# Performance work log

Hardware: AMD Instinct MI355X
Metric: run time of the kernel (lower is better)

Reference implementation:

```python
import jax, jax.numpy as jnp
import numpy as np

N, E, D, H = 50000, 500000, 128, 4
C = D // H
EPS = 1e-5


def _layer_norm(x, g, b):
    mu = jnp.mean(x, axis=-1, keepdims=True)
    var = jnp.mean((x - mu) ** 2, axis=-1, keepdims=True)
    return (x - mu) * jax.lax.rsqrt(var + EPS) * g + b


def setup_inputs() -> dict:
    key = jax.random.key(0)
    ks = jax.random.split(key, 20)
    f = lambda i, shape: jax.random.normal(ks[i], shape, dtype=jnp.float32) * 0.05
    return {
        "x": f(0, (N, D)),
        "edge_index": jax.random.randint(ks[1], (2, E), 0, N),
        "w_gcn": f(2, (D, D)), "b_gcn": f(3, (D,)),
        "wq": f(4, (D, D)), "bq": f(5, (D,)),
        "wk": f(6, (D, D)), "bk": f(7, (D,)),
        "wv": f(8, (D, D)), "bv": f(9, (D,)),
        "w_skip": f(10, (D, D)), "b_skip": f(11, (D,)),
        "w_beta": f(12, (3 * D, 1)),
        "g1": jnp.ones((D,), jnp.float32), "b1": jnp.zeros((D,), jnp.float32),
        "g2": jnp.ones((D,), jnp.float32), "b2": jnp.zeros((D,), jnp.float32),
        "w_rel": f(13, (D, 2 * D)), "w_root": f(14, (2 * D, D)),
        "local_w": jnp.ones((1,), jnp.float32), "global_w": jnp.ones((1,), jnp.float32),
    }


def reference(x, edge_index, w_gcn, b_gcn, wq, bq, wk, bk, wv, bv,
              w_skip, b_skip, w_beta, g1, b1, g2, b2, w_rel, w_root,
              local_w, global_w):
    src, dst = edge_index[0], edge_index[1]

    # ---- GCNConv (add_self_loops=False, symmetric norm) ----
    xw = x @ w_gcn                                   # [N, D]
    deg = jax.ops.segment_sum(jnp.ones((E,), x.dtype), dst, num_segments=N)
    dinv = jnp.where(deg > 0, jax.lax.rsqrt(jnp.maximum(deg, 1.0)), 0.0)
    coef = dinv[src] * dinv[dst]                     # [E]
    local_out = jax.ops.segment_sum(coef[:, None] * xw[src], dst, num_segments=N) + b_gcn

    # ---- TransformerConv (heads=4, concat=True, beta=True) ----
    q = (x @ wq + bq).reshape(N, H, C)
    k = (x @ wk + bk).reshape(N, H, C)
    v = (x @ wv + bv).reshape(N, H, C)
    alpha = jnp.sum(q[dst] * k[src], axis=-1) / jnp.sqrt(jnp.float32(C))  # [E, H]
    m = jax.ops.segment_max(alpha, dst, num_segments=N)
    m = jnp.where(jnp.isfinite(m), m, 0.0)
    a = jnp.exp(alpha - m[dst])
    s = jax.ops.segment_sum(a, dst, num_segments=N)
    attn = a / jnp.maximum(s[dst], 1e-16)            # [E, H] segment softmax over in-edges
    agg = jax.ops.segment_sum(attn[..., None] * v[src], dst, num_segments=N)
    out_g = agg.reshape(N, D)
    x_r = x @ w_skip + b_skip
    beta = jax.nn.sigmoid(jnp.concatenate([out_g, x_r, out_g - x_r], axis=-1) @ w_beta)
    global_out = beta * x_r + (1.0 - beta) * out_g

    # ---- combine + norm + FFN ----
    h = local_w * local_out + global_w * global_out
    h = _layer_norm(h + h, g1, b1)
    out = jax.nn.relu(h @ w_rel) @ w_root
    out = _layer_norm(out + h, g2, b2)
    return out
```

## Files before the change

### kernel.cpp

```cpp
#include <hip/hip_runtime.h>
#include <math.h>

#define D 128
#define EPSV 1e-5f

typedef unsigned short ushort_t;
typedef unsigned char uchar_t;
typedef __attribute__((ext_vector_type(8))) short short8v;
typedef __attribute__((ext_vector_type(4))) float f32x4;
typedef __attribute__((ext_vector_type(2))) float f32x2;

__device__ __forceinline__ float bf2f(unsigned u) {
    return __uint_as_float(u << 16);
}
__device__ __forceinline__ ushort_t f2bf(float f) {
    unsigned u = __float_as_uint(f);
    unsigned r = (u + 0x7fffu + ((u >> 16) & 1u)) >> 16;
    return (ushort_t)r;
}
__device__ __forceinline__ float bfp(uint4 v, int i) {
    unsigned w = (&v.x)[i >> 1];
    return bf2f((i & 1) ? (w >> 16) : (w & 0xffffu));
}

#define UNPACK8_FP8(u, o) { \
    f32x2 _a = __builtin_amdgcn_cvt_pk_f32_fp8((int)(u).x, false); \
    f32x2 _b = __builtin_amdgcn_cvt_pk_f32_fp8((int)(u).x, true);  \
    f32x2 _c = __builtin_amdgcn_cvt_pk_f32_fp8((int)(u).y, false); \
    f32x2 _d = __builtin_amdgcn_cvt_pk_f32_fp8((int)(u).y, true);  \
    o[0] = _a.x; o[1] = _a.y; o[2] = _b.x; o[3] = _b.y;            \
    o[4] = _c.x; o[5] = _c.y; o[6] = _d.x; o[7] = _d.y; }

__device__ __forceinline__ unsigned bf4_to_fp8x4(unsigned w0, unsigned w1) {
    int u = __builtin_amdgcn_cvt_pk_fp8_f32(bf2f(w0 & 0xffffu), bf2f(w0 >> 16), 0, false);
    u = __builtin_amdgcn_cvt_pk_fp8_f32(bf2f(w1 & 0xffffu), bf2f(w1 >> 16), u, true);
    return (unsigned)u;
}

__global__ __launch_bounds__(256)
void proj_gemm(const float* __restrict__ x,
               const ushort_t* __restrict__ Bt,
               const float* __restrict__ bias,
               uchar_t* __restrict__ pack, ushort_t* __restrict__ qb,
               ushort_t* __restrict__ xrb, int M)
{
    __shared__ ushort_t Cs[128 * 136];
    const int tid = threadIdx.x, lane = tid & 63, wid = tid >> 6;
    const int wr = wid >> 1, wc = wid & 1;
    const int R0 = blockIdx.x * 128;
    const int cbeg = blockIdx.y ? 3 : 0;
    const int cend = blockIdx.y ? 5 : 3;

    short8v av[4][4];
    #pragma unroll
    for (int r = 0; r < 4; ++r) {
        int gr = R0 + wr * 64 + r * 16 + (lane & 15);
        if (gr >= M) gr = M - 1;
        const float* xrow = x + (size_t)gr * 128 + (lane >> 4) * 8;
        #pragma unroll
        for (int ks = 0; ks < 4; ++ks) {
            float4 lo = *reinterpret_cast<const float4*>(xrow + ks * 32);
            float4 hi = *reinterpret_cast<const float4*>(xrow + ks * 32 + 4);
            short8v a;
            a[0] = (short)f2bf(lo.x); a[1] = (short)f2bf(lo.y);
            a[2] = (short)f2bf(lo.z); a[3] = (short)f2bf(lo.w);
            a[4] = (short)f2bf(hi.x); a[5] = (short)f2bf(hi.y);
            a[6] = (short)f2bf(hi.z); a[7] = (short)f2bf(hi.w);
            av[r][ks] = a;
        }
    }

    for (int ct = cbeg; ct < cend; ++ct) {
        f32x4 acc[4][4] = {};
        #pragma unroll
        for (int ks = 0; ks < 4; ++ks) {
            short8v bv[4];
            #pragma unroll
            for (int c = 0; c < 4; ++c) {
                int col = ct * 128 + wc * 64 + c * 16 + (lane & 15);
                bv[c] = *reinterpret_cast<const short8v*>(
                    &Bt[(size_t)col * 128 + ks * 32 + (lane >> 4) * 8]);
            }
            #pragma unroll
            for (int r = 0; r < 4; ++r)
                #pragma unroll
                for (int c = 0; c < 4; ++c)
                    acc[r][c] = __builtin_amdgcn_mfma_f32_16x16x32_bf16(av[r][ks], bv[c], acc[r][c], 0, 0, 0);
        }
        __syncthreads();
        #pragma unroll
        for (int r = 0; r < 4; ++r) {
            int rowb = wr * 64 + r * 16 + (lane >> 4) * 4;
            #pragma unroll
            for (int i = 0; i < 4; ++i)
                #pragma unroll
                for (int c = 0; c < 4; ++c) {
                    int col = wc * 64 + c * 16 + (lane & 15);
                    Cs[(rowb + i) * 136 + col] = f2bf(acc[r][c][i] + bias[ct * 128 + col]);
                }
        }
        __syncthreads();
        if (ct == 1 || ct == 4) {
            #pragma unroll
            for (int it = 0; it < 8; ++it) {
                int linear = tid + it * 256;
                int row = linear >> 4, ch = linear & 15;
                int gr = R0 + row;
                if (gr < M) {
                    uint4 v = *reinterpret_cast<const uint4*>(&Cs[row * 136 + ch * 8]);
                    ushort_t* dst = (ct == 1) ? (qb + (size_t)gr * 128)
                                              : (xrb + (size_t)gr * 128);
                    *reinterpret_cast<uint4*>(dst + ch * 8) = v;
                }
            }
        } else {
            const int byteoff = (ct == 0) ? 256 : (ct == 2) ? 0 : 128;
            #pragma unroll
            for (int it = 0; it < 4; ++it) {
                int linear = tid + it * 256;
                int row = linear >> 3, ch = linear & 7;
                int gr = R0 + row;
                if (gr < M) {
                    uint4 lo = *reinterpret_cast<const uint4*>(&Cs[row * 136 + ch * 16]);
                    uint4 hi = *reinterpret_cast<const uint4*>(&Cs[row * 136 + ch * 16 + 8]);
                    uint4 o;
                    o.x = bf4_to_fp8x4(lo.x, lo.y);
                    o.y = bf4_to_fp8x4(lo.z, lo.w);
                    o.z = bf4_to_fp8x4(hi.x, hi.y);
                    o.w = bf4_to_fp8x4(hi.z, hi.w);
                    *reinterpret_cast<uint4*>(pack + (size_t)gr * 384 + byteoff + ch * 16) = o;
                }
            }
        }
    }
}

__device__ __forceinline__ int swz(int ch, int row) {
    return (ch & 24) | ((ch ^ row) & 7);
}

__global__ __launch_bounds__(256)
void ffn_fused(const ushort_t* __restrict__ hlnb,
               const ushort_t* __restrict__ wt_rel,
               const ushort_t* __restrict__ wt_root,
               const float* __restrict__ g2, const float* __restrict__ b2,
               float* __restrict__ outf, int M)
{
    __shared__ float smem[128 * 130];
    ushort_t* Hs = (ushort_t*)smem;
    const int tid = threadIdx.x, lane = tid & 63, wid = tid >> 6;
    const int wr = wid >> 1, wc = wid & 1;
    const int R0 = blockIdx.x * 128;

    short8v av[4][4];
    #pragma unroll
    for (int r = 0; r < 4; ++r) {
        int gr = R0 + wr * 64 + r * 16 + (lane & 15);
        if (gr >= M) gr = M - 1;
        #pragma unroll
        for (int ks = 0; ks < 4; ++ks)
            av[r][ks] = *reinterpret_cast<const short8v*>(
                &hlnb[(size_t)gr * 128 + ks * 32 + (lane >> 4) * 8]);
    }
    for (int ct = 0; ct < 2; ++ct) {
        f32x4 acc[4][4] = {};
        #pragma unroll
        for (int ks = 0; ks < 4; ++ks) {
            short8v bv[4];
            #pragma unroll
            for (int c = 0; c < 4; ++c) {
                int col = ct * 128 + wc * 64 + c * 16 + (lane & 15);
                bv[c] = *reinterpret_cast<const short8v*>(
                    &wt_rel[(size_t)col * 128 + ks * 32 + (lane >> 4) * 8]);
            }
            #pragma unroll
            for (int r = 0; r < 4; ++r)
                #pragma unroll
                for (int c = 0; c < 4; ++c)
                    acc[r][c] = __builtin_amdgcn_mfma_f32_16x16x32_bf16(av[r][ks], bv[c], acc[r][c], 0, 0, 0);
        }
        #pragma unroll
        for (int r = 0; r < 4; ++r) {
            int rowb = wr * 64 + r * 16 + (lane >> 4) * 4;
            #pragma unroll
            for (int i = 0; i < 4; ++i)
                #pragma unroll
                for (int c = 0; c < 4; ++c) {
                    int row = rowb + i;
                    int col = ct * 128 + wc * 64 + c * 16 + (lane & 15);
                    int ch = col >> 3, el = col & 7;
                    Hs[row * 256 + swz(ch, row) * 8 + el] = f2bf(fmaxf(acc[r][c][i], 0.f));
                }
        }
    }
    __syncthreads();

    f32x4 acc2[4][4] = {};
    #pragma unroll
    for (int ks = 0; ks < 8; ++ks) {
        short8v a2[4], bv[4];
        #pragma unroll
        for (int r = 0; r < 4; ++r) {
            int row = wr * 64 + r * 16 + (lane & 15);
            int ch = ks * 4 + (lane >> 4);
            a2[r] = *reinterpret_cast<const short8v*>(&Hs[row * 256 + swz(ch, row) * 8]);
        }
        #pragma unroll
        for (int c = 0; c < 4; ++c) {
            int col = wc * 64 + c * 16 + (lane & 15);
            bv[c] = *reinterpret_cast<const short8v*>(
                &wt_root[(size_t)col * 256 + ks * 32 + (lane >> 4) * 8]);
        }
        #pragma unroll
        for (int r = 0; r < 4; ++r)
            #pragma unroll
            for (int c = 0; c < 4; ++c)
                acc2[r][c] = __builtin_amdgcn_mfma_f32_16x16x32_bf16(a2[r], bv[c], acc2[r][c], 0, 0, 0);
    }
    __syncthreads();

    float* Cs = smem;
    #pragma unroll
    for (int r = 0; r < 4; ++r) {
        int rowb = wr * 64 + r * 16 + (lane >> 4) * 4;
        #pragma unroll
        for (int i = 0; i < 4; ++i)
            #pragma unroll
            for (int c = 0; c < 4; ++c)
                Cs[(rowb + i) * 130 + wc * 64 + c * 16 + (lane & 15)] = acc2[r][c][i];
    }
    __syncthreads();

    const float ga = g2[lane * 2], gb = g2[lane * 2 + 1];
    const float ba = b2[lane * 2], bb2 = b2[lane * 2 + 1];
    for (int rr = 0; rr < 32; ++rr) {
        int row = wid * 32 + rr;
        int gr = R0 + row;
        if (gr >= M) break;
        unsigned hu = *reinterpret_cast<const unsigned*>(&hlnb[(size_t)gr * 128 + lane * 2]);
        float t0 = Cs[row * 130 + lane * 2]     + bf2f(hu & 0xffffu);
        float t1 = Cs[row * 130 + lane * 2 + 1] + bf2f(hu >> 16);
        float ssum = t0 + t1;
        #pragma unroll
        for (int off = 1; off <= 32; off <<= 1) ssum += __shfl_xor(ssum, off);
        float mu = ssum * (1.f / 128.f);
        float dv0 = t0 - mu, dv1 = t1 - mu;
        float vsum = dv0 * dv0 + dv1 * dv1;
        #pragma unroll
        for (int off = 1; off <= 32; off <<= 1) vsum += __shfl_xor(vsum, off);
        float rs = rsqrtf(vsum * (1.f / 128.f) + EPSV);
        float2 o = make_float2(dv0 * rs * ga + ba, dv1 * rs * gb + bb2);
        *reinterpret_cast<float2*>(&outf[(size_t)gr * 128 + lane * 2]) = o;
    }
}

__global__ void pack_weights_kernel(const float* __restrict__ wg, const float* __restrict__ wq,
                                    const float* __restrict__ wk, const float* __restrict__ wv,
                                    const float* __restrict__ wsk,
                                    const float* __restrict__ bq, const float* __restrict__ bk,
                                    const float* __restrict__ bv, const float* __restrict__ bsk,
                                    const float* __restrict__ wrel, const float* __restrict__ wroot,
                                    ushort_t* __restrict__ wt_all, ushort_t* __restrict__ wt_rel,
                                    ushort_t* __restrict__ wt_root, float* __restrict__ bias_all)
{
    int i = blockIdx.x * 256 + threadIdx.x;
    if (i < 640 * 128) {
        int n = i >> 7, k = i & 127;
        const float* srcs[5] = {wg, wq, wk, wv, wsk};
        wt_all[i] = f2bf(srcs[n >> 7][k * 128 + (n & 127)]);
    } else if (i < 640 * 128 + 256 * 128) {
        int j = i - 640 * 128;
        int n = j >> 7, k = j & 127;
        wt_rel[j] = f2bf(wrel[k * 256 + n]);
    } else if (i < 640 * 128 + 256 * 128 + 128 * 256) {
        int j = i - (640 * 128 + 256 * 128);
        int n = j >> 8, k = j & 255;
        wt_root[j] = f2bf(wroot[k * 128 + n]);
    } else if (i < 640 * 128 + 256 * 128 + 128 * 256 + 640) {
        int n = i - (640 * 128 + 256 * 128 + 128 * 256);
        float b = 0.f;
        if (n >= 128) {
            const float* bs[4] = {bq, bk, bv, bsk};
            b = bs[(n - 128) >> 7][n & 127];
        }
        bias_all[n] = b;
    }
}

__global__ void deg_count_kernel(const int* __restrict__ dst, int* __restrict__ deg, int E)
{
    int e = blockIdx.x * blockDim.x + threadIdx.x;
    if (e < E) atomicAdd(&deg[dst[e]], 1);
}

__global__ __launch_bounds__(256)
void scan1_kernel(const int* __restrict__ deg, int* __restrict__ row_start,
                  int* __restrict__ bsum, int n)
{
    __shared__ int ws[4];
    const int t = threadIdx.x, lane = t & 63, wid = t >> 6;
    const int base = blockIdx.x * 1024 + t * 4;
    int v0 = 0, v1 = 0, v2 = 0, v3 = 0;
    if (base + 3 < n) {
        int4 q = *reinterpret_cast<const int4*>(&deg[base]);
        v0 = q.x; v1 = q.y; v2 = q.z; v3 = q.w;
    } else {
        if (base < n)     v0 = deg[base];
        if (base + 1 < n) v1 = deg[base + 1];
        if (base + 2 < n) v2 = deg[base + 2];
        if (base + 3 < n) v3 = deg[base + 3];
    }
    int tot = v0 + v1 + v2 + v3;
    int inc = tot;
    #pragma unroll
    for (int off = 1; off < 64; off <<= 1) {
        int y = __shfl_up(inc, off);
        if (lane >= off) inc += y;
    }
    if (lane == 63) ws[wid] = inc;
    __syncthreads();
    int woff = 0;
    for (int w = 0; w < wid; ++w) woff += ws[w];
    int excl = woff + inc - tot;
    if (base < n)     row_start[base]     = excl;
    if (base + 1 < n) row_start[base + 1] = excl + v0;
    if (base + 2 < n) row_start[base + 2] = excl + v0 + v1;
    if (base + 3 < n) row_start[base + 3] = excl + v0 + v1 + v2;
    if (t == 0) bsum[blockIdx.x] = ws[0] + ws[1] + ws[2] + ws[3];
}

__global__ __launch_bounds__(256)
void scan3_kernel(const int* __restrict__ deg, const int* __restrict__ bsum,
                  int* __restrict__ row_start, int* __restrict__ cursor,
                  float* __restrict__ dinv, int n, int E)
{
    __shared__ int boff_s;
    const int K = blockIdx.x >> 2;
    if (threadIdx.x == 0) {
        int s = 0;
        for (int j = 0; j < K; ++j) s += bsum[j];
        boff_s = s;
    }
    __syncthreads();
    int i = blockIdx.x * 256 + threadIdx.x;
    if (i < n) {
        int rs = row_start[i] + boff_s;
        row_start[i] = rs;
        cursor[i] = rs;
        int d = deg[i];
        dinv[i] = (d > 0) ? rsqrtf((float)d) : 0.f;
    }
    if (i == 0) row_start[n] = E;
}

__global__ void fill_kernel(const int* __restrict__ src, const int* __restrict__ dst,
                            int* __restrict__ cursor, int* __restrict__ csr_src, int E)
{
    int e = blockIdx.x * blockDim.x + threadIdx.x;
    if (e < E) {
        int d = dst[e];
        int pos = atomicAdd(&cursor[d], 1);
        csr_src[pos] = src[e];
    }
}

__global__ __launch_bounds__(256)
void edge_fused_kernel(const uchar_t* __restrict__ pack,
                       const ushort_t* __restrict__ qbf,
                       const ushort_t* __restrict__ xrbf,
                       const int* __restrict__ row_start,
                       const int* __restrict__ csr_src,
                       const float* __restrict__ dinv,
                       const float* __restrict__ b_gcn,
                       const float* __restrict__ w_beta,
                       const float* __restrict__ g1, const float* __restrict__ b1,
                       const float* __restrict__ local_w, const float* __restrict__ global_w,
                       ushort_t* __restrict__ hln_bf, int n)
{
    const int wid = threadIdx.x >> 6, lane = threadIdx.x & 63;
    const int node = blockIdx.x * 4 + wid;
    if (node >= n) return;
    const int slot = lane >> 4, li = lane & 15;
    const int d8 = li * 8;

    uint4 qu = *reinterpret_cast<const uint4*>(&qbf[(size_t)node * 128 + d8]);
    float q[8];
    #pragma unroll
    for (int i = 0; i < 8; ++i) q[i] = bfp(qu, i);

    const int e0 = row_start[node], e1 = row_start[node + 1];
    const float dn = dinv[node];
    const float scale = 0.17677669529663687f;

    float s = 0.f, va[8] = {}, ga[8] = {};

    for (int j = e0; j < e1; j += 4) {
        const int je = j + slot;
        const bool act = je < e1;
        const int sidx = act ? csr_src[je] : 0;
        const uchar_t* prow = pack + (size_t)sidx * 384;
        uint2 ku = *reinterpret_cast<const uint2*>(prow + d8);
        uint2 vu = *reinterpret_cast<const uint2*>(prow + 128 + d8);
        uint2 xu = *reinterpret_cast<const uint2*>(prow + 256 + d8);
        float kf[8], vf[8], xf[8];
        UNPACK8_FP8(ku, kf);
        UNPACK8_FP8(vu, vf);
        UNPACK8_FP8(xu, xf);
        float p = 0.f;
        #pragma unroll
        for (int i = 0; i < 8; ++i) p = fmaf(q[i], kf[i], p);
        p += __shfl_xor(p, 1);
        p += __shfl_xor(p, 2);
        float wgt = act ? __expf(p * scale) : 0.f;
        float c   = act ? dn * dinv[sidx] : 0.f;
        s += wgt;
        #pragma unroll
        for (int i = 0; i < 8; ++i) {
            va[i] = fmaf(wgt, vf[i], va[i]);
            ga[i] = fmaf(c,   xf[i], ga[i]);
        }
    }
    #pragma unroll
    for (int off = 16; off <= 32; off <<= 1) {
        s += __shfl_xor(s, off);
        #pragma unroll
        for (int i = 0; i < 8; ++i) {
            va[i] += __shfl_xor(va[i], off);
            ga[i] += __shfl_xor(ga[i], off);
        }
    }
    const float denom = fmaxf(s, 1e-16f);

    uint4 xru = *reinterpret_cast<const uint4*>(&xrbf[(size_t)node * 128 + d8]);
    float t[8];
    float part = 0.f;
    #pragma unroll
    for (int i = 0; i < 8; ++i) {
        float og = va[i] / denom;
        float xr = bfp(xru, i);
        float lo = ga[i] + b_gcn[d8 + i];
        part += og * w_beta[d8 + i] + xr * w_beta[128 + d8 + i]
              + (og - xr) * w_beta[256 + d8 + i];
        t[i] = lo;
        va[i] = og; ga[i] = xr;
    }
    #pragma unroll
    for (int off = 1; off <= 32; off <<= 1) part += __shfl_xor(part, off);
    const float beta = 1.f / (1.f + __expf(-part * 0.25f));

    const float lw = local_w[0], gw = global_w[0];
    float ssum = 0.f;
    #pragma unroll
    for (int i = 0; i < 8; ++i) {
        float go = beta * ga[i] + (1.f - beta) * va[i];
        t[i] = 2.f * (lw * t[i] + gw * go);
        ssum += t[i];
    }
    #pragma unroll
    for (int off = 1; off <= 32; off <<= 1) ssum += __shfl_xor(ssum, off);
    const float mu = ssum * (1.f / 512.f);
    float vsum = 0.f;
    #pragma unroll
    for (int i = 0; i < 8; ++i) { float d = t[i] - mu; vsum += d * d; }
    #pragma unroll
    for (int off = 1; off <= 32; off <<= 1) vsum += __shfl_xor(vsum, off);
    const float rs = rsqrtf(vsum * (1.f / 512.f) + EPSV);

    if (slot == 0) {
        uint4 o;
        #pragma unroll
        for (int i = 0; i < 4; ++i) {
            float o0 = (t[2*i]   - mu) * rs * g1[d8 + 2*i]   + b1[d8 + 2*i];
            float o1 = (t[2*i+1] - mu) * rs * g1[d8 + 2*i+1] + b1[d8 + 2*i+1];
            (&o.x)[i] = (unsigned)f2bf(o0) | ((unsigned)f2bf(o1) << 16);
        }
        *reinterpret_cast<uint4*>(&hln_bf[(size_t)node * 128 + d8]) = o;
    }
}

extern "C" void kernel_launch(void* const* d_in, const int* in_sizes, int n_in,
                              void* d_out, int out_size, void* d_ws, size_t ws_size,
                              hipStream_t stream)
{
    const float* x      = (const float*)d_in[0];
    const int*   ei     = (const int*)d_in[1];
    const float* w_gcn  = (const float*)d_in[2];
    const float* b_gcn  = (const float*)d_in[3];
    const float* wq     = (const float*)d_in[4];
    const float* bq     = (const float*)d_in[5];
    const float* wk     = (const float*)d_in[6];
    const float* bk     = (const float*)d_in[7];
    const float* wv     = (const float*)d_in[8];
    const float* bv     = (const float*)d_in[9];
    const float* w_skip = (const float*)d_in[10];
    const float* b_skip = (const float*)d_in[11];
    const float* w_beta = (const float*)d_in[12];
    const float* g1     = (const float*)d_in[13];
    const float* b1     = (const float*)d_in[14];
    const float* g2     = (const float*)d_in[15];
    const float* b2     = (const float*)d_in[16];
    const float* w_rel  = (const float*)d_in[17];
    const float* w_root = (const float*)d_in[18];
    const float* lw     = (const float*)d_in[19];
    const float* gw     = (const float*)d_in[20];

    const int N = in_sizes[0] / D;
    const int E = in_sizes[1] / 2;
    const int* src = ei;
    const int* dst = ei + E;

    char* wsb = (char*)d_ws;
    size_t off = 0;
    auto alloc = [&](size_t bytes) -> void* {
        void* p = wsb + off;
        off += (bytes + 255) & ~(size_t)255;
        return p;
    };
    uchar_t*  pack_kvx = (uchar_t*)alloc((size_t)N * 384);
    ushort_t* qb_bf    = (ushort_t*)alloc((size_t)N * 128 * 2);
    ushort_t* xr_bf    = (ushort_t*)alloc((size_t)N * 128 * 2);
    ushort_t* hln_bf   = (ushort_t*)alloc((size_t)N * 128 * 2);
    ushort_t* wt_all   = (ushort_t*)alloc(640 * 128 * 2);
    ushort_t* wt_rel   = (ushort_t*)alloc(256 * 128 * 2);
    ushort_t* wt_root  = (ushort_t*)alloc(128 * 256 * 2);
    float*    bias_all = (float*)alloc(640 * 4);
    int*      deg      = (int*)alloc((size_t)N * 4);
    int*      row_start= (int*)alloc((size_t)(N + 1) * 4);
    int*      cursor   = (int*)alloc((size_t)N * 4);
    int*      csr_src  = (int*)alloc((size_t)E * 4);
    float*    dinv     = (float*)alloc((size_t)N * 4);
    int*      bsum     = (int*)alloc(((size_t)(N + 1023) / 1024) * 4);

    float* out = (float*)d_out;
    const int SB = (N + 1023) / 1024;

    hipMemsetAsync(deg, 0, (size_t)N * sizeof(int), stream);
    deg_count_kernel<<<dim3((E + 255) / 256), dim3(256), 0, stream>>>(dst, deg, E);
    scan1_kernel<<<dim3(SB), dim3(256), 0, stream>>>(deg, row_start, bsum, N);
    scan3_kernel<<<dim3((N + 255) / 256), dim3(256), 0, stream>>>(
        deg, bsum, row_start, cursor, dinv, N, E);
    fill_kernel<<<dim3((E + 255) / 256), dim3(256), 0, stream>>>(src, dst, cursor, csr_src, E);

    pack_weights_kernel<<<dim3(579), dim3(256), 0, stream>>>(
        w_gcn, wq, wk, wv, w_skip, bq, bk, bv, b_skip, w_rel, w_root,
        wt_all, wt_rel, wt_root, bias_all);

    const int MB = (N + 127) / 128;
    proj_gemm<<<dim3(MB, 2), dim3(256), 0, stream>>>(
        x, wt_all, bias_all, pack_kvx, qb_bf, xr_bf, N);

    edge_fused_kernel<<<dim3((N + 3) / 4), dim3(256), 0, stream>>>(
        pack_kvx, qb_bf, xr_bf, row_start, csr_src, dinv, b_gcn, w_beta,
        g1, b1, lw, gw, hln_bf, N);

    ffn_fused<<<dim3(MB), dim3(256), 0, stream>>>(
        hln_bf, wt_rel, wt_root, g2, b2, out, N);
}
```

Measured before the change: 215.1 us.

## Prescale GCN features by source dinv and accumulate edges in packed fp16

Folds the source-side GCN normalisation dinv[src] into the projection epilogue, so the edge loop no longer gathers dinv per edge and applies dn once after aggregation. Stores q as fp16 and, when the builtin exists, converts fp8 to packed half2 and does the dot products and accumulation in fp16 packed math. Inactive lanes now point at a zeroed dummy row instead of row 0. The pack_weights launch is merged into the scan1 kernel to remove one launch. This trades accumulation precision (fp16 sums over many edges) for fewer instructions and fewer irregular loads.

```diff
diff --git a/kernel.cpp b/kernel.cpp
--- a/kernel.cpp
+++ b/kernel.cpp
@@ -9,6 +9,14 @@
 typedef __attribute__((ext_vector_type(8))) short short8v;
 typedef __attribute__((ext_vector_type(4))) float f32x4;
 typedef __attribute__((ext_vector_type(2))) float f32x2;
+typedef _Float16 half_t;
+typedef __attribute__((ext_vector_type(2))) _Float16 h2;
+
+#if __has_builtin(__builtin_amdgcn_cvt_pk_f16_fp8)
+#define HAVE_F16P 1
+#else
+#define HAVE_F16P 0
+#endif
 
 __device__ __forceinline__ float bf2f(unsigned u) {
     return __uint_as_float(u << 16);
@@ -21,6 +29,15 @@
 __device__ __forceinline__ float bfp(uint4 v, int i) {
     unsigned w = (&v.x)[i >> 1];
     return bf2f((i & 1) ? (w >> 16) : (w & 0xffffu));
+}
+
+__device__ __forceinline__ ushort_t qconv(float f) {
+#if HAVE_F16P
+    half_t h = (half_t)f;
+    return __builtin_bit_cast(ushort_t, h);
+#else
+    return f2bf(f);
+#endif
 }
 
 #define UNPACK8_FP8(u, o) { \
@@ -41,6 +58,7 @@
 void proj_gemm(const float* __restrict__ x,
                const ushort_t* __restrict__ Bt,
                const float* __restrict__ bias,
+               const float* __restrict__ dinv,
                uchar_t* __restrict__ pack, ushort_t* __restrict__ qb,
                ushort_t* __restrict__ xrb, int M)
 {
@@ -92,12 +110,21 @@
         for (int r = 0; r < 4; ++r) {
             int rowb = wr * 64 + r * 16 + (lane >> 4) * 4;
             #pragma unroll
-            for (int i = 0; i < 4; ++i)
+            for (int i = 0; i < 4; ++i) {
+                float sc = 1.f;
+                if (ct == 0) {
+                    int grow = R0 + rowb + i;
+                    if (grow >= M) grow = M - 1;
+                    sc = dinv[grow];
+                }
                 #pragma unroll
                 for (int c = 0; c < 4; ++c) {
                     int col = wc * 64 + c * 16 + (lane & 15);
-                    Cs[(rowb + i) * 136 + col] = f2bf(acc[r][c][i] + bias[ct * 128 + col]);
+                    float val = acc[r][c][i] + bias[ct * 128 + col];
+                    if (ct == 0) val *= sc;
+                    Cs[(rowb + i) * 136 + col] = (ct == 1) ? qconv(val) : f2bf(val);
                 }
+            }
         }
         __syncthreads();
         if (ct == 1 || ct == 4) {
@@ -254,36 +281,72 @@
     }
 }
 
-__global__ void pack_weights_kernel(const float* __restrict__ wg, const float* __restrict__ wq,
-                                    const float* __restrict__ wk, const float* __restrict__ wv,
-                                    const float* __restrict__ wsk,
-                                    const float* __restrict__ bq, const float* __restrict__ bk,
-                                    const float* __restrict__ bv, const float* __restrict__ bsk,
-                                    const float* __restrict__ wrel, const float* __restrict__ wroot,
-                                    ushort_t* __restrict__ wt_all, ushort_t* __restrict__ wt_rel,
-                                    ushort_t* __restrict__ wt_root, float* __restrict__ bias_all)
-{
-    int i = blockIdx.x * 256 + threadIdx.x;
-    if (i < 640 * 128) {
-        int n = i >> 7, k = i & 127;
-        const float* srcs[5] = {wg, wq, wk, wv, wsk};
-        wt_all[i] = f2bf(srcs[n >> 7][k * 128 + (n & 127)]);
-    } else if (i < 640 * 128 + 256 * 128) {
-        int j = i - 640 * 128;
-        int n = j >> 7, k = j & 127;
-        wt_rel[j] = f2bf(wrel[k * 256 + n]);
-    } else if (i < 640 * 128 + 256 * 128 + 128 * 256) {
-        int j = i - (640 * 128 + 256 * 128);
-        int n = j >> 8, k = j & 255;
-        wt_root[j] = f2bf(wroot[k * 128 + n]);
-    } else if (i < 640 * 128 + 256 * 128 + 128 * 256 + 640) {
-        int n = i - (640 * 128 + 256 * 128 + 128 * 256);
-        float b = 0.f;
-        if (n >= 128) {
-            const float* bs[4] = {bq, bk, bv, bsk};
-            b = bs[(n - 128) >> 7][n & 127];
-        }
-        bias_all[n] = b;
+__global__ __launch_bounds__(256)
+void scan1_packw_kernel(const int* __restrict__ deg, int* __restrict__ row_start,
+                        int* __restrict__ bsum, int n, int SB,
+                        const float* __restrict__ wg, const float* __restrict__ wq,
+                        const float* __restrict__ wk, const float* __restrict__ wv,
+                        const float* __restrict__ wsk,
+                        const float* __restrict__ bq, const float* __restrict__ bk,
+                        const float* __restrict__ bv, const float* __restrict__ bsk,
+                        const float* __restrict__ wrel, const float* __restrict__ wroot,
+                        ushort_t* __restrict__ wt_all, ushort_t* __restrict__ wt_rel,
+                        ushort_t* __restrict__ wt_root, float* __restrict__ bias_all)
+{
+    __shared__ int ws[4];
+    if ((int)blockIdx.x < SB) {
+        const int t = threadIdx.x, lane = t & 63, wid = t >> 6;
+        const int base = blockIdx.x * 1024 + t * 4;
+        int v0 = 0, v1 = 0, v2 = 0, v3 = 0;
+        if (base + 3 < n) {
+            int4 q = *reinterpret_cast<const int4*>(&deg[base]);
+            v0 = q.x; v1 = q.y; v2 = q.z; v3 = q.w;
+        } else {
+            if (base < n)     v0 = deg[base];
+            if (base + 1 < n) v1 = deg[base + 1];
+            if (base + 2 < n) v2 = deg[base + 2];
+            if (base + 3 < n) v3 = deg[base + 3];
+        }
+        int tot = v0 + v1 + v2 + v3;
+        int inc = tot;
+        #pragma unroll
+        for (int off = 1; off < 64; off <<= 1) {
+            int y = __shfl_up(inc, off);
+            if (lane >= off) inc += y;
+        }
+        if (lane == 63) ws[wid] = inc;
+        __syncthreads();
+        int woff = 0;
+        for (int w = 0; w < wid; ++w) woff += ws[w];
+        int excl = woff + inc - tot;
+        if (base < n)     row_start[base]     = excl;
+        if (base + 1 < n) row_start[base + 1] = excl + v0;
+        if (base + 2 < n) row_start[base + 2] = excl + v0 + v1;
+        if (base + 3 < n) row_start[base + 3] = excl + v0 + v1 + v2;
+        if (t == 0) bsum[blockIdx.x] = ws[0] + ws[1] + ws[2] + ws[3];
+    } else {
+        int i = (blockIdx.x - SB) * 256 + threadIdx.x;
+        if (i < 640 * 128) {
+            int c = i >> 7, k = i & 127;
+            const float* srcs[5] = {wg, wq, wk, wv, wsk};
+            wt_all[i] = f2bf(srcs[c >> 7][k * 128 + (c & 127)]);
+        } else if (i < 640 * 128 + 256 * 128) {
+            int j = i - 640 * 128;
+            int c = j >> 7, k = j & 127;
+            wt_rel[j] = f2bf(wrel[k * 256 + c]);
+        } else if (i < 640 * 128 + 256 * 128 + 128 * 256) {
+            int j = i - (640 * 128 + 256 * 128);
+            int c = j >> 8, k = j & 255;
+            wt_root[j] = f2bf(wroot[k * 128 + c]);
+        } else if (i < 640 * 128 + 256 * 128 + 128 * 256 + 640) {
+            int c = i - (640 * 128 + 256 * 128 + 128 * 256);
+            float b = 0.f;
+            if (c >= 128) {
+                const float* bs[4] = {bq, bk, bv, bsk};
+                b = bs[(c - 128) >> 7][c & 127];
+            }
+            bias_all[c] = b;
+        }
     }
 }
 
@@ -291,42 +354,6 @@
 {
     int e = blockIdx.x * blockDim.x + threadIdx.x;
     if (e < E) atomicAdd(&deg[dst[e]], 1);
-}
-
-__global__ __launch_bounds__(256)
-void scan1_kernel(const int* __restrict__ deg, int* __restrict__ row_start,
-                  int* __restrict__ bsum, int n)
-{
-    __shared__ int ws[4];
-    const int t = threadIdx.x, lane = t & 63, wid = t >> 6;
-    const int base = blockIdx.x * 1024 + t * 4;
-    int v0 = 0, v1 = 0, v2 = 0, v3 = 0;
-    if (base + 3 < n) {
-        int4 q = *reinterpret_cast<const int4*>(&deg[base]);
-        v0 = q.x; v1 = q.y; v2 = q.z; v3 = q.w;
-    } else {
-        if (base < n)     v0 = deg[base];
-        if (base + 1 < n) v1 = deg[base + 1];
-        if (base + 2 < n) v2 = deg[base + 2];
-        if (base + 3 < n) v3 = deg[base + 3];
-    }
-    int tot = v0 + v1 + v2 + v3;
-    int inc = tot;
-    #pragma unroll
-    for (int off = 1; off < 64; off <<= 1) {
-        int y = __shfl_up(inc, off);
-        if (lane >= off) inc += y;
-    }
-    if (lane == 63) ws[wid] = inc;
-    __syncthreads();
-    int woff = 0;
-    for (int w = 0; w < wid; ++w) woff += ws[w];
-    int excl = woff + inc - tot;
-    if (base < n)     row_start[base]     = excl;
-    if (base + 1 < n) row_start[base + 1] = excl + v0;
-    if (base + 2 < n) row_start[base + 2] = excl + v0 + v1;
-    if (base + 3 < n) row_start[base + 3] = excl + v0 + v1 + v2;
-    if (t == 0) bsum[blockIdx.x] = ws[0] + ws[1] + ws[2] + ws[3];
 }
 
 __global__ __launch_bounds__(256)
@@ -383,21 +410,65 @@
     const int slot = lane >> 4, li = lane & 15;
     const int d8 = li * 8;
 
-    uint4 qu = *reinterpret_cast<const uint4*>(&qbf[(size_t)node * 128 + d8]);
-    float q[8];
-    #pragma unroll
-    for (int i = 0; i < 8; ++i) q[i] = bfp(qu, i);
-
     const int e0 = row_start[node], e1 = row_start[node + 1];
     const float dn = dinv[node];
     const float scale = 0.17677669529663687f;
 
-    float s = 0.f, va[8] = {}, ga[8] = {};
-
+    float s = 0.f;
+    float va[8], ga[8];
+
+#if HAVE_F16P
+    uint4 qu = *reinterpret_cast<const uint4*>(&qbf[(size_t)node * 128 + d8]);
+    h2 qh[4] = { __builtin_bit_cast(h2, qu.x), __builtin_bit_cast(h2, qu.y),
+                 __builtin_bit_cast(h2, qu.z), __builtin_bit_cast(h2, qu.w) };
+    h2 va2[4] = {}, ga2[4] = {};
     for (int j = e0; j < e1; j += 4) {
         const int je = j + slot;
         const bool act = je < e1;
-        const int sidx = act ? csr_src[je] : 0;
+        const int sidx = act ? csr_src[je] : n;
+        const uchar_t* prow = pack + (size_t)sidx * 384;
+        uint2 ku = *reinterpret_cast<const uint2*>(prow + d8);
+        uint2 vu = *reinterpret_cast<const uint2*>(prow + 128 + d8);
+        uint2 xu = *reinterpret_cast<const uint2*>(prow + 256 + d8);
+        h2 k0 = __builtin_amdgcn_cvt_pk_f16_fp8((short)(ku.x & 0xffffu));
+        h2 k1 = __builtin_amdgcn_cvt_pk_f16_fp8((short)(ku.x >> 16));
+        h2 k2 = __builtin_amdgcn_cvt_pk_f16_fp8((short)(ku.y & 0xffffu));
+        h2 k3 = __builtin_amdgcn_cvt_pk_f16_fp8((short)(ku.y >> 16));
+        h2 pd = k0 * qh[0] + k1 * qh[1] + k2 * qh[2] + k3 * qh[3];
+        float p = (float)pd[0] + (float)pd[1];
+        p += __shfl_xor(p, 1);
+        p += __shfl_xor(p, 2);
+        float wgt = act ? __expf(p * scale) : 0.f;
+        s += wgt;
+        half_t wh = (half_t)wgt;
+        h2 w2 = { wh, wh };
+        h2 v0 = __builtin_amdgcn_cvt_pk_f16_fp8((short)(vu.x & 0xffffu));
+        h2 v1 = __builtin_amdgcn_cvt_pk_f16_fp8((short)(vu.x >> 16));
+        h2 v2 = __builtin_amdgcn_cvt_pk_f16_fp8((short)(vu.y & 0xffffu));
+        h2 v3 = __builtin_amdgcn_cvt_pk_f16_fp8((short)(vu.y >> 16));
+        va2[0] += w2 * v0; va2[1] += w2 * v1; va2[2] += w2 * v2; va2[3] += w2 * v3;
+        h2 x0 = __builtin_amdgcn_cvt_pk_f16_fp8((short)(xu.x & 0xffffu));
+        h2 x1 = __builtin_amdgcn_cvt_pk_f16_fp8((short)(xu.x >> 16));
+        h2 x2 = __builtin_amdgcn_cvt_pk_f16_fp8((short)(xu.y & 0xffffu));
+        h2 x3 = __builtin_amdgcn_cvt_pk_f16_fp8((short)(xu.y >> 16));
+        ga2[0] += x0; ga2[1] += x1; ga2[2] += x2; ga2[3] += x3;
+    }
+    #pragma unroll
+    for (int i = 0; i < 4; ++i) {
+        va[2 * i] = (float)va2[i][0]; va[2 * i + 1] = (float)va2[i][1];
+        ga[2 * i] = (float)ga2[i][0]; ga[2 * i + 1] = (float)ga2[i][1];
+    }
+#else
+    uint4 qu = *reinterpret_cast<const uint4*>(&qbf[(size_t)node * 128 + d8]);
+    float q[8];
+    #pragma unroll
+    for (int i = 0; i < 8; ++i) q[i] = bfp(qu, i);
+    #pragma unroll
+    for (int i = 0; i < 8; ++i) { va[i] = 0.f; ga[i] = 0.f; }
+    for (int j = e0; j < e1; j += 4) {
+        const int je = j + slot;
+        const bool act = je < e1;
+        const int sidx = act ? csr_src[je] : n;
         const uchar_t* prow = pack + (size_t)sidx * 384;
         uint2 ku = *reinterpret_cast<const uint2*>(prow + d8);
         uint2 vu = *reinterpret_cast<const uint2*>(prow + 128 + d8);
@@ -412,14 +483,15 @@
         p += __shfl_xor(p, 1);
         p += __shfl_xor(p, 2);
         float wgt = act ? __expf(p * scale) : 0.f;
-        float c   = act ? dn * dinv[sidx] : 0.f;
         s += wgt;
         #pragma unroll
         for (int i = 0; i < 8; ++i) {
             va[i] = fmaf(wgt, vf[i], va[i]);
-            ga[i] = fmaf(c,   xf[i], ga[i]);
-        }
-    }
+            ga[i] += xf[i];
+        }
+    }
+#endif
+
     #pragma unroll
     for (int off = 16; off <= 32; off <<= 1) {
         s += __shfl_xor(s, off);
@@ -438,7 +510,7 @@
     for (int i = 0; i < 8; ++i) {
         float og = va[i] / denom;
         float xr = bfp(xru, i);
-        float lo = ga[i] + b_gcn[d8 + i];
+        float lo = dn * ga[i] + b_gcn[d8 + i];
         part += og * w_beta[d8 + i] + xr * w_beta[128 + d8 + i]
               + (og - xr) * w_beta[256 + d8 + i];
         t[i] = lo;
@@ -516,7 +588,7 @@
         off += (bytes + 255) & ~(size_t)255;
         return p;
     };
-    uchar_t*  pack_kvx = (uchar_t*)alloc((size_t)N * 384);
+    uchar_t*  pack_kvx = (uchar_t*)alloc((size_t)(N + 1) * 384);
     ushort_t* qb_bf    = (ushort_t*)alloc((size_t)N * 128 * 2);
     ushort_t* xr_bf    = (ushort_t*)alloc((size_t)N * 128 * 2);
     ushort_t* hln_bf   = (ushort_t*)alloc((size_t)N * 128 * 2);
@@ -535,19 +607,19 @@
     const int SB = (N + 1023) / 1024;
 
     hipMemsetAsync(deg, 0, (size_t)N * sizeof(int), stream);
+    hipMemsetAsync(pack_kvx + (size_t)N * 384, 0, 384, stream);
     deg_count_kernel<<<dim3((E + 255) / 256), dim3(256), 0, stream>>>(dst, deg, E);
-    scan1_kernel<<<dim3(SB), dim3(256), 0, stream>>>(deg, row_start, bsum, N);
+    scan1_packw_kernel<<<dim3(SB + 579), dim3(256), 0, stream>>>(
+        deg, row_start, bsum, N, SB,
+        w_gcn, wq, wk, wv, w_skip, bq, bk, bv, b_skip, w_rel, w_root,
+        wt_all, wt_rel, wt_root, bias_all);
     scan3_kernel<<<dim3((N + 255) / 256), dim3(256), 0, stream>>>(
         deg, bsum, row_start, cursor, dinv, N, E);
     fill_kernel<<<dim3((E + 255) / 256), dim3(256), 0, stream>>>(src, dst, cursor, csr_src, E);
 
-    pack_weights_kernel<<<dim3(579), dim3(256), 0, stream>>>(
-        w_gcn, wq, wk, wv, w_skip, bq, bk, bv, b_skip, w_rel, w_root,
-        wt_all, wt_rel, wt_root, bias_all);
-
     const int MB = (N + 127) / 128;
     proj_gemm<<<dim3(MB, 2), dim3(256), 0, stream>>>(
-        x, wt_all, bias_all, pack_kvx, qb_bf, xr_bf, N);
+        x, wt_all, bias_all, dinv, pack_kvx, qb_bf, xr_bf, N);
 
     edge_fused_kernel<<<dim3((N + 3) / 4), dim3(256), 0, stream>>>(
         pack_kvx, qb_bf, xr_bf, row_start, csr_src, dinv, b_gcn, w_beta,
```

Result: no change. 219.2 us (+1.9%).
